# Kernel optimization log

Measured on AMD Instinct MI355X. Metric: run time of the kernel, lower is better.

Reference implementation:

```python
import jax, jax.numpy as jnp
import numpy as np

M_FIELDS = 26   # cin_size[0]
H1 = 128        # cin_size[1]
H2 = 128        # cin_size[2]
BATCH = 2048
EMB_K = 32


def setup_inputs() -> dict:
    key = jax.random.key(0)
    k0, k1, k2, k3, k4 = jax.random.split(key, 5)
    inputs = jax.random.normal(k0, (BATCH, M_FIELDS, EMB_K), dtype=jnp.float32)
    # Conv3d(1, H1, kernel=(26,26,1)) -> weight [H1, H_prev=26, m=26], bias [H1]
    W1 = jax.random.normal(k1, (H1, M_FIELDS, M_FIELDS), dtype=jnp.float32) * 0.05
    b1 = jax.random.normal(k2, (H1,), dtype=jnp.float32) * 0.05
    # Conv3d(1, H2, kernel=(H1,26,1)) -> weight [H2, H1, m=26], bias [H2]
    W2 = jax.random.normal(k3, (H2, H1, M_FIELDS), dtype=jnp.float32) * 0.05
    b2 = jax.random.normal(k4, (H2,), dtype=jnp.float32) * 0.05
    return {"inputs": inputs, "W1": W1, "b1": b1, "W2": W2, "b2": b2}


def _cin_layer(x_prev, x0, W, b):
    # x_prev: [B, H_prev, k], x0: [B, m, k], W: [H, H_prev, m], b: [H]
    # Equivalent to: outer product z[b,i,j,k] = x_prev[b,i,k]*x0[b,j,k],
    # then Conv3d with kernel (H_prev, m, 1): out[b,h,k] = sum_ij W[h,i,j]*z + b[h]
    return jnp.einsum('bik,bjk,hij->bhk', x_prev, x0, W) + b[None, :, None]


def reference(inputs, W1, b1, W2, b2):
    x1 = _cin_layer(inputs, inputs, W1, b1)   # [B, H1, k]
    x2 = _cin_layer(x1, inputs, W2, b2)       # [B, H2, k]
    res = jnp.concatenate([x1, x2], axis=1)   # [B, H1+H2, k]
    return jnp.sum(res, axis=-1)              # [B, H1+H2]
```

## Files before the change

### kernel.cpp

```cpp
#include <hip/hip_runtime.h>

typedef __bf16 bf16;
typedef __bf16 bf16x8 __attribute__((ext_vector_type(8)));
typedef __bf16 bf16x4 __attribute__((ext_vector_type(4)));
typedef float f32x4 __attribute__((ext_vector_type(4)));
typedef unsigned int u32;

#define NB    2048
#define NM    26
#define NJP   27

__device__ __forceinline__ void gl_lds16(const bf16* g, bf16* l) {
  __builtin_amdgcn_global_load_lds(
      (const __attribute__((address_space(1))) void*)g,
      (__attribute__((address_space(3))) void*)l, 16, 0, 0);
}

__global__ __launch_bounds__(256) void prep_all(
    const float* __restrict__ W1, const float* __restrict__ W2,
    bf16* __restrict__ w1t, bf16* __restrict__ w2t2)
{
  const int bid = blockIdx.x, t = threadIdx.x;
  #pragma unroll
  for (int g = 0; g < 4; ++g) {
    int ge = g*160768 + bid*256 + t;
    if (ge < 110592) {
      int e = ge;
      int el = e & 7, lr = (e >> 3) & 15, lq = (e >> 7) & 3, ni = (e >> 9) & 3;
      int rest = e >> 11;
      int c = rest % NJP, cs_idx = rest / NJP;
      int h = cs_idx*64 + ni*16 + lr;
      int i = lq*8 + el;
      float v = (i < NM && c < NM) ? W1[h*(NM*NM) + i*NM + c] : 0.f;
      w1t[e] = (bf16)v;
    } else {
      int e = ge - 110592;
      int el = e & 7, lr = (e >> 3) & 15, lq = (e >> 7) & 3, ni = (e >> 9) & 3;
      int rest = e >> 11;
      int kc = rest % 130, cs_idx = rest / 130;
      int h = cs_idx*64 + ni*16 + lr;
      int c = lq*8 + el;
      float v = (kc < 128 && c < NM) ? W2[h*(128*NM) + kc*NM + c] : 0.f;
      w2t2[e] = (bf16)v;
    }
  }
}

#define STEP(CUR, NXT, J) do {                                                 \
  { int jn = ((J)+1 > 25) ? 25 : (J)+1;         \
    scf[NXT][0][0] = spw0[jn*32];  scf[NXT][0][1] = spw0[jn*32 + 16];          \
    scf[NXT][1][0] = spw1[jn*32];  scf[NXT][1][1] = spw1[jn*32 + 16]; }        \
  _Pragma("unroll")                                                            \
  for (int ni = 0; ni < 4; ++ni)                                               \
    B[NXT][ni] = *(const bf16x8*)(tb + (long)((J)+1)*2048 + ni*512);           \
  _Pragma("unroll")                                                            \
  for (int bb = 0; bb < 2; ++bb)                                               \
    _Pragma("unroll")                                                          \
    for (int mi = 0; mi < 2; ++mi) {                                           \
      bf16x8 af;                                                               \
      _Pragma("unroll")                                                        \
      for (int e = 0; e < 8; ++e)                                              \
        af[e] = (bf16)(xf32[bb][mi][e] * scf[CUR][bb][mi]);                    \
      _Pragma("unroll")                                                        \
      for (int ni = 0; ni < 4; ++ni)                                           \
        acc[bb][mi][ni] = __builtin_amdgcn_mfma_f32_16x16x32_bf16(af,          \
                                    B[CUR][ni], acc[bb][mi][ni], 0, 0, 0);     \
    }                                                                          \
} while (0)

__global__ __launch_bounds__(256, 2) void cin1G(
    const float* __restrict__ in, const bf16* __restrict__ w1t,
    const float* __restrict__ b1, bf16* __restrict__ G2, float* __restrict__ out)
{
  __shared__ __align__(16) bf16 ldsT[4][64*36];
  const int t = threadIdx.x, bid = blockIdx.x;
  const int lane = t & 63, w = t >> 6;
  const int lr = lane & 15, lq = lane >> 4;
  const int fo = lq*128 + lr*8;
  const int cs_idx = bid & 1, cs = cs_idx * 64;
  const int strip8 = bid >> 1;
  const int bw0 = strip8*8 + w*2;

  const float* bin0 = in + (long)bw0*(NM*32);
  const float* bin1 = bin0 + NM*32;
  const float* spw0 = bin0 + lr;
  const float* spw1 = bin1 + lr;

  float xf32[2][2][8];
  #pragma unroll
  for (int bb = 0; bb < 2; ++bb) {
    const float* bin = bb ? bin1 : bin0;
    #pragma unroll
    for (int mi = 0; mi < 2; ++mi)
      #pragma unroll
      for (int e = 0; e < 8; ++e) {
        int j = lq*8 + e;
        xf32[bb][mi][e] = (j < NM) ? bin[j*32 + mi*16 + lr] : 0.f;
      }
  }

  f32x4 acc[2][2][4];
  #pragma unroll
  for (int bb=0; bb<2; ++bb)
    #pragma unroll
    for (int mi=0; mi<2; ++mi)
      #pragma unroll
      for (int ni=0; ni<4; ++ni) acc[bb][mi][ni] = {0.f,0.f,0.f,0.f};

  const bf16* tb = w1t + (long)cs_idx*NJP*2048 + fo;

  float scf[2][2][2];
  bf16x8 B[2][4];
  #pragma unroll
  for (int ni = 0; ni < 4; ++ni)
    B[0][ni] = *(const bf16x8*)(tb + ni*512);
  scf[0][0][0] = spw0[0];  scf[0][0][1] = spw0[16];
  scf[0][1][0] = spw1[0];  scf[0][1][1] = spw1[16];

  for (int jj = 0; jj < 13; ++jj) {
    STEP(0, 1, 2*jj);
    STEP(1, 0, 2*jj + 1);
  }

  float bias[4];
  #pragma unroll
  for (int ni=0; ni<4; ++ni) bias[ni] = b1[cs + ni*16 + lr];

  bf16* T = &ldsT[w][0];

  #pragma unroll
  for (int bb = 0; bb < 2; ++bb) {
    const int bw = bw0 + bb;
    const float* bin = bb ? bin1 : bin0;

    #pragma unroll
    for (int ni=0; ni<4; ++ni) {
      float vv = 0.f;
      #pragma unroll
      for (int mi=0; mi<2; ++mi)
        #pragma unroll
        for (int r=0; r<4; ++r) vv += acc[bb][mi][ni][r];
      vv += __shfl_xor(vv, 16, 64);
      vv += __shfl_xor(vv, 32, 64);
      if (lq == 0) out[bw*256 + cs + ni*16 + lr] = vv + 32.0f * bias[ni];
    }

    #pragma unroll
    for (int mi=0; mi<2; ++mi)
      #pragma unroll
      for (int ni=0; ni<4; ++ni) {
        bf16x4 pk;
        #pragma unroll
        for (int r=0; r<4; ++r) pk[r] = (bf16)(acc[bb][mi][ni][r] + bias[ni]);
        *(bf16x4*)&T[(ni*16+lr)*36 + mi*16 + lq*4] = pk;
      }

    bf16x8 bg[2];
    #pragma unroll
    for (int nt = 0; nt < 2; ++nt) {
      int j = nt*16 + lr;
      bf16x8 vv;
      #pragma unroll
      for (int e=0; e<8; ++e) vv[e] = (bf16)0.f;
      if (j < NM) {
        const float* src = bin + j*32 + lq*8;
        f32x4 a = *(const f32x4*)src, c = *(const f32x4*)(src+4);
        #pragma unroll
        for (int e=0; e<4; ++e) { vv[e] = (bf16)a[e]; vv[4+e] = (bf16)c[e]; }
      }
      bg[nt] = vv;
    }
    const long gbase = (long)(bw >> 5)*131072 + (bw & 31)*8;
    #pragma unroll
    for (int mt = 0; mt < 4; ++mt) {
      bf16x8 ag = *(const bf16x8*)&T[(mt*16+lr)*36 + lq*8];
      #pragma unroll
      for (int nt = 0; nt < 2; ++nt) {
        f32x4 z = {0.f,0.f,0.f,0.f};
        f32x4 g = __builtin_amdgcn_mfma_f32_16x16x32_bf16(bg[nt], ag, z, 0, 0, 0);
        bf16x4 pk;
        #pragma unroll
        for (int r = 0; r < 4; ++r) pk[r] = (bf16)g[r];
        const int kh = (cs + mt*16 + lr)*4 + nt*2 + (lq >> 1);
        *(bf16x4*)&G2[gbase + (long)kh*256 + (lq & 1)*4] = pk;
      }
    }
  }
}

#define STEPG(CUR, NXT, KREL) do {                                             \
  A[NXT] = *(const bf16x8*)(Ab + (long)(kc0 + (KREL) + 1)*1024);               \
  _Pragma("unroll")                                                            \
  for (int ni = 0; ni < 4; ++ni) {                                             \
    bf16x8 bfr = *(const bf16x8*)&ldsW[(KREL)*2048 + ni*512 + fo];             \
    acc[ni] = __builtin_amdgcn_mfma_f32_16x16x32_bf16(A[CUR], bfr,             \
                                                      acc[ni], 0, 0, 0);       \
  }                                                                            \
} while (0)

__global__ __launch_bounds__(256, 2) void gemm2(
    const bf16* __restrict__ G2, const bf16* __restrict__ w2t2,
    const float* __restrict__ b2, float* __restrict__ out)
{
  __shared__ __align__(16) bf16 ldsW[16*2048];
  const int t = threadIdx.x, bid = blockIdx.x;
  const int lane = t & 63, w = t >> 6;
  const int lr = lane & 15, lq = lane >> 4;
  const int fo = lq*128 + lr*8;
  const int s = bid & 7;
  const int csx = (bid >> 3) & 1;
  const int g = bid >> 4;
  const int ms16 = g*4 + w;
  const int ms32 = ms16 >> 1, mif = ms16 & 1;
  const int kc0 = s*16;

  {
    const bf16* src = w2t2 + ((long)csx*130 + kc0)*2048;
    #pragma unroll
    for (int i = 0; i < 16; ++i)
      gl_lds16(src + i*2048 + t*8, &ldsW[i*2048 + t*8]);
  }
  __syncthreads();

  const bf16* Ab = G2 + (long)ms32*131072 + mif*128 + lq*256 + lr*8;

  f32x4 acc[4];
  #pragma unroll
  for (int ni=0; ni<4; ++ni) acc[ni] = {0.f,0.f,0.f,0.f};

  bf16x8 A[2];
  A[0] = *(const bf16x8*)(Ab + (long)kc0*1024);

  for (int jj = 0; jj < 8; ++jj) {
    STEPG(0, 1, 2*jj);
    STEPG(1, 0, 2*jj + 1);
  }

  if (s == 0) {
    #pragma unroll
    for (int ni=0; ni<4; ++ni) {
      float bv = 32.0f * b2[csx*64 + ni*16 + lr];
      #pragma unroll
      for (int r=0; r<4; ++r) acc[ni][r] += bv;
    }
  }

  #pragma unroll
  for (int ni=0; ni<4; ++ni) {
    int h = csx*64 + ni*16 + lr;
    #pragma unroll
    for (int r=0; r<4; ++r) {
      int b = ms16*16 + lq*4 + r;
      atomicAdd(&out[b*256 + 128 + h], acc[ni][r]);
    }
  }
}

extern "C" void kernel_launch(void* const* d_in, const int* in_sizes, int n_in,
                              void* d_out, int out_size, void* d_ws, size_t ws_size,
                              hipStream_t stream) {
  const float* in = (const float*)d_in[0];
  const float* W1 = (const float*)d_in[1];
  const float* b1 = (const float*)d_in[2];
  const float* W2 = (const float*)d_in[3];
  const float* b2 = (const float*)d_in[4];
  float* out = (float*)d_out;

  char* ws = (char*)d_ws;
  bf16* w1t  = (bf16*)(ws);
  bf16* w2t2 = (bf16*)(ws + 1048576);
  bf16* G2   = (bf16*)(ws + 4194304);

  prep_all<<<628, 256, 0, stream>>>(W1, W2, w1t, w2t2);
  cin1G  <<<512, 256, 0, stream>>>(in, w1t, b1, G2, out);
  gemm2  <<<512, 256, 0, stream>>>(G2, w2t2, b2, out);
}
```

Before: 102.0 us.

## Fuse layer-2 GEMM into layer-1 kernel via LDS-staged intermediate

```diff
diff --git a/kernel.cpp b/kernel.cpp
--- a/kernel.cpp
+++ b/kernel.cpp
@@ -9,12 +9,6 @@
 #define NB    2048
 #define NM    26
 #define NJP   27
-
-__device__ __forceinline__ void gl_lds16(const bf16* g, bf16* l) {
-  __builtin_amdgcn_global_load_lds(
-      (const __attribute__((address_space(1))) void*)g,
-      (__attribute__((address_space(3))) void*)l, 16, 0, 0);
-}
 
 __global__ __launch_bounds__(256) void prep_all(
     const float* __restrict__ W1, const float* __restrict__ W2,
@@ -68,18 +62,30 @@
     }                                                                          \
 } while (0)
 
-__global__ __launch_bounds__(256, 2) void cin1G(
+#define STEPM(CUR, NXT, KL) do {                                               \
+  Af[NXT] = *(const bf16x8*)&ldsG[(((KL)+1)*4 + lq)*72 + lr*8];                \
+  Bf[NXT][0] = *(const bf16x8*)(Bb0 + (long)((KL)+1)*2048);                    \
+  Bf[NXT][1] = *(const bf16x8*)(Bb1 + (long)((KL)+1)*2048);                    \
+  _Pragma("unroll")                                                            \
+  for (int ht = 0; ht < 2; ++ht)                                               \
+    acc2[ht] = __builtin_amdgcn_mfma_f32_16x16x32_bf16(Af[CUR], Bf[CUR][ht],   \
+                                                       acc2[ht], 0, 0, 0);     \
+} while (0)
+
+__global__ __launch_bounds__(256, 2) void cinfuse(
     const float* __restrict__ in, const bf16* __restrict__ w1t,
-    const float* __restrict__ b1, bf16* __restrict__ G2, float* __restrict__ out)
+    const bf16* __restrict__ w2t2, const float* __restrict__ b1,
+    const float* __restrict__ b2, float* __restrict__ out)
 {
   __shared__ __align__(16) bf16 ldsT[4][64*36];
+  __shared__ __align__(16) bf16 ldsG[264*72];
   const int t = threadIdx.x, bid = blockIdx.x;
   const int lane = t & 63, w = t >> 6;
   const int lr = lane & 15, lq = lane >> 4;
   const int fo = lq*128 + lr*8;
   const int cs_idx = bid & 1, cs = cs_idx * 64;
-  const int strip8 = bid >> 1;
-  const int bw0 = strip8*8 + w*2;
+  const int grp = bid >> 1;
+  const int bw0 = grp*8 + w*2;
 
   const float* bin0 = in + (long)bw0*(NM*32);
   const float* bin1 = bin0 + NM*32;
@@ -131,6 +137,7 @@
   #pragma unroll
   for (int bb = 0; bb < 2; ++bb) {
     const int bw = bw0 + bb;
+    const int bloc = w*2 + bb;
     const float* bin = bb ? bin1 : bin0;
 
     #pragma unroll
@@ -170,7 +177,6 @@
       }
       bg[nt] = vv;
     }
-    const long gbase = (long)(bw >> 5)*131072 + (bw & 31)*8;
     #pragma unroll
     for (int mt = 0; mt < 4; ++mt) {
       bf16x8 ag = *(const bf16x8*)&T[(mt*16+lr)*36 + lq*8];
@@ -181,77 +187,49 @@
         bf16x4 pk;
         #pragma unroll
         for (int r = 0; r < 4; ++r) pk[r] = (bf16)g[r];
-        const int kh = (cs + mt*16 + lr)*4 + nt*2 + (lq >> 1);
-        *(bf16x4*)&G2[gbase + (long)kh*256 + (lq & 1)*4] = pk;
-      }
-    }
-  }
-}
-
-#define STEPG(CUR, NXT, KREL) do {                                             \
-  A[NXT] = *(const bf16x8*)(Ab + (long)(kc0 + (KREL) + 1)*1024);               \
-  _Pragma("unroll")                                                            \
-  for (int ni = 0; ni < 4; ++ni) {                                             \
-    bf16x8 bfr = *(const bf16x8*)&ldsW[(KREL)*2048 + ni*512 + fo];             \
-    acc[ni] = __builtin_amdgcn_mfma_f32_16x16x32_bf16(A[CUR], bfr,             \
-                                                      acc[ni], 0, 0, 0);       \
-  }                                                                            \
-} while (0)
-
-__global__ __launch_bounds__(256, 2) void gemm2(
-    const bf16* __restrict__ G2, const bf16* __restrict__ w2t2,
-    const float* __restrict__ b2, float* __restrict__ out)
-{
-  __shared__ __align__(16) bf16 ldsW[16*2048];
-  const int t = threadIdx.x, bid = blockIdx.x;
-  const int lane = t & 63, w = t >> 6;
-  const int lr = lane & 15, lq = lane >> 4;
-  const int fo = lq*128 + lr*8;
-  const int s = bid & 7;
-  const int csx = (bid >> 3) & 1;
-  const int g = bid >> 4;
-  const int ms16 = g*4 + w;
-  const int ms32 = ms16 >> 1, mif = ms16 & 1;
-  const int kc0 = s*16;
-
-  {
-    const bf16* src = w2t2 + ((long)csx*130 + kc0)*2048;
-    #pragma unroll
-    for (int i = 0; i < 16; ++i)
-      gl_lds16(src + i*2048 + t*8, &ldsW[i*2048 + t*8]);
-  }
+        const int kh = (mt*16 + lr)*4 + nt*2 + (lq >> 1);
+        *(bf16x4*)&ldsG[kh*72 + bloc*8 + (lq & 1)*4] = pk;
+      }
+    }
+  }
+
   __syncthreads();
 
-  const bf16* Ab = G2 + (long)ms32*131072 + mif*128 + lq*256 + lr*8;
-
-  f32x4 acc[4];
-  #pragma unroll
-  for (int ni=0; ni<4; ++ni) acc[ni] = {0.f,0.f,0.f,0.f};
-
-  bf16x8 A[2];
-  A[0] = *(const bf16x8*)(Ab + (long)kc0*1024);
-
-  for (int jj = 0; jj < 8; ++jj) {
-    STEPG(0, 1, 2*jj);
-    STEPG(1, 0, 2*jj + 1);
-  }
-
-  if (s == 0) {
-    #pragma unroll
-    for (int ni=0; ni<4; ++ni) {
-      float bv = 32.0f * b2[csx*64 + ni*16 + lr];
-      #pragma unroll
-      for (int r=0; r<4; ++r) acc[ni][r] += bv;
-    }
-  }
-
-  #pragma unroll
-  for (int ni=0; ni<4; ++ni) {
-    int h = csx*64 + ni*16 + lr;
-    #pragma unroll
-    for (int r=0; r<4; ++r) {
-      int b = ms16*16 + lq*4 + r;
-      atomicAdd(&out[b*256 + 128 + h], acc[ni][r]);
+  const int ht0 = w*2, ht1 = w*2 + 1;
+  const bf16* Bb0 = w2t2 + ((long)(ht0 >> 2)*130 + cs)*2048 + (ht0 & 3)*512 + fo;
+  const bf16* Bb1 = w2t2 + ((long)(ht1 >> 2)*130 + cs)*2048 + (ht1 & 3)*512 + fo;
+
+  f32x4 acc2[2];
+  acc2[0] = {0.f,0.f,0.f,0.f};  acc2[1] = {0.f,0.f,0.f,0.f};
+
+  bf16x8 Af[2], Bf[2][2];
+  Af[0] = *(const bf16x8*)&ldsG[lq*72 + lr*8];
+  Bf[0][0] = *(const bf16x8*)Bb0;
+  Bf[0][1] = *(const bf16x8*)Bb1;
+
+  for (int jj = 0; jj < 32; ++jj) {
+    STEPM(0, 1, 2*jj);
+    STEPM(1, 0, 2*jj + 1);
+  }
+
+  if (cs_idx == 0) {
+    #pragma unroll
+    for (int ht = 0; ht < 2; ++ht) {
+      float bv = 32.0f * b2[(w*2 + ht)*16 + lr];
+      #pragma unroll
+      for (int r=0; r<4; ++r) acc2[ht][r] += bv;
+    }
+  }
+
+  if (lq < 2) {
+    #pragma unroll
+    for (int ht = 0; ht < 2; ++ht) {
+      int h = (w*2 + ht)*16 + lr;
+      #pragma unroll
+      for (int r=0; r<4; ++r) {
+        int b = grp*8 + lq*4 + r;
+        atomicAdd(&out[b*256 + 128 + h], acc2[ht][r]);
+      }
     }
   }
 }
@@ -269,9 +247,7 @@
   char* ws = (char*)d_ws;
   bf16* w1t  = (bf16*)(ws);
   bf16* w2t2 = (bf16*)(ws + 1048576);
-  bf16* G2   = (bf16*)(ws + 4194304);
 
   prep_all<<<628, 256, 0, stream>>>(W1, W2, w1t, w2t2);
-  cin1G  <<<512, 256, 0, stream>>>(in, w1t, b1, G2, out);
-  gemm2  <<<512, 256, 0, stream>>>(G2, w2t2, b2, out);
+  cinfuse <<<512, 256, 0, stream>>>(in, w1t, w2t2, b1, b2, out);
 }
```

After: 95.19 us. 6.7% less time.
